# Optimization experiments

Measured on AMD Instinct MI355X. Metric: run time of the kernel, lower is better.

The kernel has to match this reference:

```python
import jax, jax.numpy as jnp
import numpy as np

M, D, I, E, TOPK = 2048, 1024, 2048, 8, 2

def setup_inputs() -> dict:
    key = jax.random.key(0)
    k1, k2, k3, k4 = jax.random.split(key, 4)
    x = jax.random.normal(k1, (M, D), dtype=jnp.float32)
    w13 = jax.random.normal(k2, (E, 2 * I, D), dtype=jnp.float32) * 0.02
    w2 = jax.random.normal(k3, (E, D, I), dtype=jnp.float32) * 0.02
    expert_indices = jax.random.randint(k4, (M, TOPK), 0, E, dtype=jnp.int64)
    return {"x": x, "w13": w13, "w2": w2, "expert_indices": expert_indices}

def reference(x, w13, w2, expert_indices):
    # Faithful to the 'gpt-fast' math: per (token, slot) SiLU-gated expert FFN.
    # Instead of gathering per-token weight copies (huge), compute each expert's
    # FFN densely over all tokens, then gather the selected expert output.
    inter = w2.shape[2]

    def per_expert(w13_e, w2_e):
        h = jnp.einsum('md,nd->mn', x, w13_e)          # [M, 2I]
        x1, x3 = h[:, :inter], h[:, inter:]
        return jnp.einsum('mi,di->md', jax.nn.silu(x1) * x3, w2_e)  # [M, D]

    outs = jax.vmap(per_expert)(w13, w2)               # [E, M, D]
    outs = jnp.transpose(outs, (1, 0, 2))              # [M, E, D]
    # out[t, a] = outs[t, expert_indices[t, a]]
    idx = expert_indices[..., None]                    # [M, TOPK, 1]
    return jnp.take_along_axis(outs, idx, axis=1)      # [M, TOPK, D]
```

## Files before the change

### kernel.cpp

```cpp
#include <hip/hip_runtime.h>
#include <hip/hip_bf16.h>
#include <cstdint>
#include <cstddef>

#define DDIM  1024
#define IDIM  2048
#define NEXP  8
#define NPAIR 4096
#define KSPLIT 2
#define MAXTILE 40

typedef __attribute__((ext_vector_type(8))) short short8;
typedef __attribute__((ext_vector_type(4))) float floatx4;

__device__ inline short8 pack8(float4 a, float4 b) {
    union { short8 s8; __hip_bfloat162 h[4]; } u;
    u.h[0] = __float22bfloat162_rn(float2{a.x, a.y});
    u.h[1] = __float22bfloat162_rn(float2{a.z, a.w});
    u.h[2] = __float22bfloat162_rn(float2{b.x, b.y});
    u.h[3] = __float22bfloat162_rn(float2{b.z, b.w});
    return u.s8;
}

__device__ inline void gload_lds16(const unsigned short* g, unsigned short* l) {
    __builtin_amdgcn_global_load_lds((const __attribute__((address_space(1))) void*)g,
                                     (__attribute__((address_space(3))) void*)l, 16, 0, 0);
}

__global__ void cvt_all(const float4* __restrict__ x, const float4* __restrict__ w13,
                        const float4* __restrict__ w2,
                        uint4* __restrict__ xb, uint4* __restrict__ w13b,
                        uint4* __restrict__ w2b) {
    const int i = blockIdx.x * 256 + threadIdx.x;
    const int NX   = (2048 * 1024) / 8;
    const int NW13 = (8 * 4096 * 1024) / 8;
    const float4* src; uint4* dst; int j;
    if (i < NX)              { src = x;   dst = xb;   j = i; }
    else if (i < NX + NW13)  { src = w13; dst = w13b; j = i - NX; }
    else                     { src = w2;  dst = w2b;  j = i - NX - NW13; }
    float4 a = src[2 * j], b = src[2 * j + 1];
    short8 p = pack8(a, b);
    dst[j] = *(uint4*)&p;
}

__global__ void route_kernel(const int* __restrict__ eidx,
                             int4* __restrict__ tbl,
                             int* __restrict__ slot_q) {
    __shared__ int cnt[NEXP];
    __shared__ int base[NEXP];
    __shared__ int cur[NEXP];
    const int t = threadIdx.x;
    if (t < NEXP) cnt[t] = 0;
    __syncthreads();
    for (int q = t; q < NPAIR; q += 1024) atomicAdd(&cnt[eidx[q]], 1);
    __syncthreads();
    if (t == 0) {
        int s = 0, nt = 0;
        for (int e = 0; e < NEXP; e++) {
            base[e] = s; cur[e] = s;
            for (int mb = 0; mb < cnt[e]; mb += 128)
                tbl[nt++] = int4{e, mb, s, cnt[e]};
            s += cnt[e];
        }
        for (; nt < MAXTILE; nt++) tbl[nt] = int4{0, 0, 0, 0};
    }
    __syncthreads();
    for (int q = t; q < NPAIR; q += 1024) {
        int e = eidx[q];
        int pos = atomicAdd(&cur[e], 1);
        slot_q[pos] = q;
    }
}

__launch_bounds__(256)
__global__ void gemm1_swiglu(const unsigned short* __restrict__ xb,
                             const unsigned short* __restrict__ w13b,
                             const int4* __restrict__ tbl,
                             const int* __restrict__ slot_q,
                             unsigned short* __restrict__ pbuf) {
    const int4 tt = tbl[blockIdx.y];
    const int e = tt.x, mbase = tt.y, off0 = tt.z, ne = tt.w;
    if (mbase >= ne) return;
    const int n0 = blockIdx.x * 64;

    __shared__ __align__(16) unsigned short As[128 * 32];
    __shared__ __align__(16) unsigned short Bs[128 * 32];

    const int t    = threadIdx.x;
    const int lane = t & 63;
    const int wid  = t >> 6;

    const int r0 = t >> 2;
    const int sg = (t & 3) ^ (r0 & 3);
    int slA0 = mbase + r0;      if (slA0 > ne - 1) slA0 = ne - 1;
    int slA1 = mbase + r0 + 64; if (slA1 > ne - 1) slA1 = ne - 1;
    const unsigned short* pA0 = xb + (size_t)(slot_q[off0 + slA0] >> 1) * DDIM + sg * 8;
    const unsigned short* pA1 = xb + (size_t)(slot_q[off0 + slA1] >> 1) * DDIM + sg * 8;
    const unsigned short* wbase = w13b + (size_t)e * (2 * IDIM) * DDIM;
    const unsigned short* pB0 = wbase + (size_t)(n0 + r0) * DDIM + sg * 8;
    const unsigned short* pB1 = wbase + (size_t)(IDIM + n0 + r0) * DDIM + sg * 8;
    unsigned short* lA0 = As + wid * 512;
    unsigned short* lA1 = As + 2048 + wid * 512;
    unsigned short* lB0 = Bs + wid * 512;
    unsigned short* lB1 = Bs + 2048 + wid * 512;

    const int wm = wid >> 1, wn = wid & 1;
    const int quad = lane >> 4, l16 = lane & 15;
    const int swz = (quad ^ (l16 & 3)) * 8;

    floatx4 acc1[4][2], acc3[4][2];
    #pragma unroll
    for (int i = 0; i < 4; i++)
        #pragma unroll
        for (int j = 0; j < 2; j++) {
            acc1[i][j] = floatx4{0.f, 0.f, 0.f, 0.f};
            acc3[i][j] = floatx4{0.f, 0.f, 0.f, 0.f};
        }

    for (int it = 0; it < DDIM / 32; ++it) {
        const int ko = it * 32;
        __syncthreads();
        gload_lds16(pA0 + ko, lA0);
        gload_lds16(pA1 + ko, lA1);
        gload_lds16(pB0 + ko, lB0);
        gload_lds16(pB1 + ko, lB1);
        __syncthreads();

        short8 af[4], b1f[2], b3f[2];
        #pragma unroll
        for (int mi = 0; mi < 4; mi++)
            af[mi] = *(short8*)&As[(wm * 64 + mi * 16 + l16) * 32 + swz];
        #pragma unroll
        for (int ni = 0; ni < 2; ni++) {
            b1f[ni] = *(short8*)&Bs[(wn * 32 + ni * 16 + l16) * 32 + swz];
            b3f[ni] = *(short8*)&Bs[(64 + wn * 32 + ni * 16 + l16) * 32 + swz];
        }
        #pragma unroll
        for (int mi = 0; mi < 4; mi++)
            #pragma unroll
            for (int ni = 0; ni < 2; ni++) {
                acc1[mi][ni] = __builtin_amdgcn_mfma_f32_16x16x32_bf16(af[mi], b1f[ni], acc1[mi][ni], 0, 0, 0);
                acc3[mi][ni] = __builtin_amdgcn_mfma_f32_16x16x32_bf16(af[mi], b3f[ni], acc3[mi][ni], 0, 0, 0);
            }
    }

    #pragma unroll
    for (int mi = 0; mi < 4; mi++) {
        #pragma unroll
        for (int ni = 0; ni < 2; ni++) {
            const int col = n0 + wn * 32 + ni * 16 + l16;
            #pragma unroll
            for (int rr = 0; rr < 4; rr++) {
                const int s2 = mbase + wm * 64 + mi * 16 + quad * 4 + rr;
                if (s2 < ne) {
                    float v1 = acc1[mi][ni][rr];
                    float v3 = acc3[mi][ni][rr];
                    float pv = v1 / (1.f + __expf(-v1)) * v3;
                    __hip_bfloat16 pb = __float2bfloat16(pv);
                    pbuf[(size_t)(off0 + s2) * IDIM + col] = *(unsigned short*)&pb;
                }
            }
        }
    }
}

__launch_bounds__(256)
__global__ void gemm2_scatter(const unsigned short* __restrict__ pbuf,
                              const unsigned short* __restrict__ w2b,
                              const int4* __restrict__ tbl,
                              const int* __restrict__ slot_q,
                              float* __restrict__ out,
                              float* __restrict__ p1) {
    const int4 tt = tbl[blockIdx.y];
    const int e = tt.x, mbase = tt.y, off0 = tt.z, ne = tt.w;
    if (mbase >= ne) return;
    const int n0 = blockIdx.x * 128;
    const int ks = blockIdx.z;
    const int kbase = ks * (IDIM / KSPLIT);

    __shared__ __align__(16) unsigned short As[128 * 32];
    __shared__ __align__(16) unsigned short Bs[128 * 32];

    const int t    = threadIdx.x;
    const int lane = t & 63;
    const int wid  = t >> 6;

    const int r0 = t >> 2;
    const int sg = (t & 3) ^ (r0 & 3);
    int slA0 = mbase + r0;      if (slA0 > ne - 1) slA0 = ne - 1;
    int slA1 = mbase + r0 + 64; if (slA1 > ne - 1) slA1 = ne - 1;
    const unsigned short* pA0 = pbuf + (size_t)(off0 + slA0) * IDIM + kbase + sg * 8;
    const unsigned short* pA1 = pbuf + (size_t)(off0 + slA1) * IDIM + kbase + sg * 8;
    const unsigned short* wbase = w2b + (size_t)e * DDIM * IDIM;
    const unsigned short* pB0 = wbase + (size_t)(n0 + r0) * IDIM + kbase + sg * 8;
    const unsigned short* pB1 = wbase + (size_t)(n0 + 64 + r0) * IDIM + kbase + sg * 8;
    unsigned short* lA0 = As + wid * 512;
    unsigned short* lA1 = As + 2048 + wid * 512;
    unsigned short* lB0 = Bs + wid * 512;
    unsigned short* lB1 = Bs + 2048 + wid * 512;

    const int wm = wid >> 1, wn = wid & 1;
    const int quad = lane >> 4, l16 = lane & 15;
    const int swz = (quad ^ (l16 & 3)) * 8;

    floatx4 acc[4][4];
    #pragma unroll
    for (int i = 0; i < 4; i++)
        #pragma unroll
        for (int j = 0; j < 4; j++) acc[i][j] = floatx4{0.f, 0.f, 0.f, 0.f};

    for (int it = 0; it < (IDIM / KSPLIT) / 32; ++it) {
        const int ko = it * 32;
        __syncthreads();
        gload_lds16(pA0 + ko, lA0);
        gload_lds16(pA1 + ko, lA1);
        gload_lds16(pB0 + ko, lB0);
        gload_lds16(pB1 + ko, lB1);
        __syncthreads();

        short8 af[4], bf[4];
        #pragma unroll
        for (int mi = 0; mi < 4; mi++)
            af[mi] = *(short8*)&As[(wm * 64 + mi * 16 + l16) * 32 + swz];
        #pragma unroll
        for (int ni = 0; ni < 4; ni++)
            bf[ni] = *(short8*)&Bs[(wn * 64 + ni * 16 + l16) * 32 + swz];
        #pragma unroll
        for (int mi = 0; mi < 4; mi++)
            #pragma unroll
            for (int ni = 0; ni < 4; ni++)
                acc[mi][ni] = __builtin_amdgcn_mfma_f32_16x16x32_bf16(af[mi], bf[ni], acc[mi][ni], 0, 0, 0);
    }

    float* dstbase = (ks == 0) ? out : p1;
    #pragma unroll
    for (int mi = 0; mi < 4; mi++) {
        #pragma unroll
        for (int rr = 0; rr < 4; rr++) {
            const int s2 = mbase + wm * 64 + mi * 16 + quad * 4 + rr;
            if (s2 < ne) {
                const int qq = slot_q[off0 + s2];
                float* orow = dstbase + (size_t)qq * DDIM;
                #pragma unroll
                for (int ni = 0; ni < 4; ni++)
                    orow[n0 + wn * 64 + ni * 16 + l16] = acc[mi][ni][rr];
            }
        }
    }
}

__global__ void reduce_add(float4* __restrict__ out, const float4* __restrict__ p1) {
    const int i = blockIdx.x * 256 + threadIdx.x;
    float4 a = out[i], b = p1[i];
    out[i] = float4{a.x + b.x, a.y + b.y, a.z + b.z, a.w + b.w};
}

extern "C" void kernel_launch(void* const* d_in, const int* in_sizes, int n_in,
                              void* d_out, int out_size, void* d_ws, size_t ws_size,
                              hipStream_t stream) {
    const float* x    = (const float*)d_in[0];
    const float* w13  = (const float*)d_in[1];
    const float* w2   = (const float*)d_in[2];
    const int*   eidx = (const int*)d_in[3];
    float* out = (float*)d_out;

    const size_t OFF_XB   = 65536;
    const size_t OFF_W13B = OFF_XB + (size_t)4 * 1024 * 1024;
    const size_t OFF_W2B  = OFF_W13B + (size_t)64 * 1024 * 1024;
    const size_t OFF_PBUF = OFF_W2B + (size_t)32 * 1024 * 1024;

    int4* tbl   = (int4*)((char*)d_ws + 128);
    int* slot_q = (int*)((char*)d_ws + 1024);
    unsigned short* xb   = (unsigned short*)((char*)d_ws + OFF_XB);
    unsigned short* w13b = (unsigned short*)((char*)d_ws + OFF_W13B);
    unsigned short* w2b  = (unsigned short*)((char*)d_ws + OFF_W2B);
    unsigned short* pbuf = (unsigned short*)((char*)d_ws + OFF_PBUF);
    float* p1 = (float*)((char*)d_ws + OFF_W13B);

    hipLaunchKernelGGL(cvt_all, dim3(25600), dim3(256), 0, stream,
                       (const float4*)x, (const float4*)w13, (const float4*)w2,
                       (uint4*)xb, (uint4*)w13b, (uint4*)w2b);
    hipLaunchKernelGGL(route_kernel, dim3(1), dim3(1024), 0, stream, eidx, tbl, slot_q);
    hipLaunchKernelGGL(gemm1_swiglu, dim3(IDIM / 64, MAXTILE), dim3(256), 0, stream,
                       xb, w13b, tbl, slot_q, pbuf);
    hipLaunchKernelGGL(gemm2_scatter, dim3(DDIM / 128, MAXTILE, KSPLIT), dim3(256), 0, stream,
                       pbuf, w2b, tbl, slot_q, out, p1);
    hipLaunchKernelGGL(reduce_add, dim3((NPAIR * DDIM / 4) / 256), dim3(256), 0, stream,
                       (float4*)out, (const float4*)p1);
}
```

Before: 386.2 us.

## Double K-tile depth, raise gemm2 split-K to four, grid-stride nontemporal conversion

Both GEMMs now stage 64-wide K slices per barrier pair instead of 32, with an 8-way XOR swizzle, halving the number of sync/load rounds. The gemm2 split-K goes from 2 to 4 with all partials written to a scratch buffer and summed by a four-way reduce kernel. The fp32-to-bf16 conversion becomes a grid-stride loop with nontemporal loads and two packs per thread, and routing is launched before conversion. The risk is more LDS per block, which lowers occupancy, plus extra partial-sum traffic in the reduce.

```diff
diff --git a/kernel.cpp b/kernel.cpp
--- a/kernel.cpp
+++ b/kernel.cpp
@@ -7,11 +7,12 @@
 #define IDIM  2048
 #define NEXP  8
 #define NPAIR 4096
-#define KSPLIT 2
+#define KSPLIT 4
 #define MAXTILE 40
 
 typedef __attribute__((ext_vector_type(8))) short short8;
 typedef __attribute__((ext_vector_type(4))) float floatx4;
+typedef __attribute__((ext_vector_type(4))) float fvec4;
 
 __device__ inline short8 pack8(float4 a, float4 b) {
     union { short8 s8; __hip_bfloat162 h[4]; } u;
@@ -22,32 +23,49 @@
     return u.s8;
 }
 
+__device__ inline short8 pack8v(fvec4 a, fvec4 b) {
+    union { short8 s8; __hip_bfloat162 h[4]; } u;
+    u.h[0] = __float22bfloat162_rn(float2{a.x, a.y});
+    u.h[1] = __float22bfloat162_rn(float2{a.z, a.w});
+    u.h[2] = __float22bfloat162_rn(float2{b.x, b.y});
+    u.h[3] = __float22bfloat162_rn(float2{b.z, b.w});
+    return u.s8;
+}
+
 __device__ inline void gload_lds16(const unsigned short* g, unsigned short* l) {
     __builtin_amdgcn_global_load_lds((const __attribute__((address_space(1))) void*)g,
                                      (__attribute__((address_space(3))) void*)l, 16, 0, 0);
 }
 
-__global__ void cvt_all(const float4* __restrict__ x, const float4* __restrict__ w13,
-                        const float4* __restrict__ w2,
+__global__ void cvt_all(const fvec4* __restrict__ x, const fvec4* __restrict__ w13,
+                        const fvec4* __restrict__ w2,
                         uint4* __restrict__ xb, uint4* __restrict__ w13b,
                         uint4* __restrict__ w2b) {
-    const int i = blockIdx.x * 256 + threadIdx.x;
     const int NX   = (2048 * 1024) / 8;
     const int NW13 = (8 * 4096 * 1024) / 8;
-    const float4* src; uint4* dst; int j;
-    if (i < NX)              { src = x;   dst = xb;   j = i; }
-    else if (i < NX + NW13)  { src = w13; dst = w13b; j = i - NX; }
-    else                     { src = w2;  dst = w2b;  j = i - NX - NW13; }
-    float4 a = src[2 * j], b = src[2 * j + 1];
-    short8 p = pack8(a, b);
-    dst[j] = *(uint4*)&p;
+    const int NW2  = (8 * 1024 * 2048) / 8;
+    const int total2 = (NX + NW13 + NW2) / 2;
+    for (int i2 = blockIdx.x * 256 + threadIdx.x; i2 < total2; i2 += gridDim.x * 256) {
+        const int i = 2 * i2;
+        const fvec4* src; uint4* dst; int j;
+        if (i < NX)              { src = x;   dst = xb;   j = i; }
+        else if (i < NX + NW13)  { src = w13; dst = w13b; j = i - NX; }
+        else                     { src = w2;  dst = w2b;  j = i - NX - NW13; }
+        fvec4 a0 = __builtin_nontemporal_load(src + 2 * j + 0);
+        fvec4 a1 = __builtin_nontemporal_load(src + 2 * j + 1);
+        fvec4 a2 = __builtin_nontemporal_load(src + 2 * j + 2);
+        fvec4 a3 = __builtin_nontemporal_load(src + 2 * j + 3);
+        short8 p0 = pack8v(a0, a1);
+        short8 p1 = pack8v(a2, a3);
+        dst[j]     = *(uint4*)&p0;
+        dst[j + 1] = *(uint4*)&p1;
+    }
 }
 
 __global__ void route_kernel(const int* __restrict__ eidx,
                              int4* __restrict__ tbl,
                              int* __restrict__ slot_q) {
     __shared__ int cnt[NEXP];
-    __shared__ int base[NEXP];
     __shared__ int cur[NEXP];
     const int t = threadIdx.x;
     if (t < NEXP) cnt[t] = 0;
@@ -57,7 +75,7 @@
     if (t == 0) {
         int s = 0, nt = 0;
         for (int e = 0; e < NEXP; e++) {
-            base[e] = s; cur[e] = s;
+            cur[e] = s;
             for (int mb = 0; mb < cnt[e]; mb += 128)
                 tbl[nt++] = int4{e, mb, s, cnt[e]};
             s += cnt[e];
@@ -83,30 +101,34 @@
     if (mbase >= ne) return;
     const int n0 = blockIdx.x * 64;
 
-    __shared__ __align__(16) unsigned short As[128 * 32];
-    __shared__ __align__(16) unsigned short Bs[128 * 32];
+    __shared__ __align__(16) unsigned short As[128 * 64];
+    __shared__ __align__(16) unsigned short Bs[128 * 64];
 
     const int t    = threadIdx.x;
     const int lane = t & 63;
     const int wid  = t >> 6;
 
-    const int r0 = t >> 2;
-    const int sg = (t & 3) ^ (r0 & 3);
-    int slA0 = mbase + r0;      if (slA0 > ne - 1) slA0 = ne - 1;
-    int slA1 = mbase + r0 + 64; if (slA1 > ne - 1) slA1 = ne - 1;
-    const unsigned short* pA0 = xb + (size_t)(slot_q[off0 + slA0] >> 1) * DDIM + sg * 8;
-    const unsigned short* pA1 = xb + (size_t)(slot_q[off0 + slA1] >> 1) * DDIM + sg * 8;
-    const unsigned short* wbase = w13b + (size_t)e * (2 * IDIM) * DDIM;
-    const unsigned short* pB0 = wbase + (size_t)(n0 + r0) * DDIM + sg * 8;
-    const unsigned short* pB1 = wbase + (size_t)(IDIM + n0 + r0) * DDIM + sg * 8;
-    unsigned short* lA0 = As + wid * 512;
-    unsigned short* lA1 = As + 2048 + wid * 512;
-    unsigned short* lB0 = Bs + wid * 512;
-    unsigned short* lB1 = Bs + 2048 + wid * 512;
+    const int rr = t >> 3;
+    const int g  = (t & 7) ^ (rr & 7);
+    const unsigned short* pA[4];
+    const unsigned short* pB[4];
+    const unsigned short* wb1 = w13b + (size_t)e * (2 * IDIM) * DDIM;
+    #pragma unroll
+    for (int c = 0; c < 4; c++) {
+        int row = c * 32 + rr;
+        int sl = mbase + row; if (sl > ne - 1) sl = ne - 1;
+        pA[c] = xb + (size_t)(slot_q[off0 + sl] >> 1) * DDIM + g * 8;
+        int wrow = (row < 64) ? (n0 + row) : (IDIM + n0 + (row - 64));
+        pB[c] = wb1 + (size_t)wrow * DDIM + g * 8;
+    }
+    unsigned short* lA = As + wid * 512;
+    unsigned short* lB = Bs + wid * 512;
 
     const int wm = wid >> 1, wn = wid & 1;
     const int quad = lane >> 4, l16 = lane & 15;
-    const int swz = (quad ^ (l16 & 3)) * 8;
+    const int rsw = l16 & 7;
+    const int co0 = (quad ^ rsw) * 8;
+    const int co1 = ((quad + 4) ^ rsw) * 8;
 
     floatx4 acc1[4][2], acc3[4][2];
     #pragma unroll
@@ -117,31 +139,36 @@
             acc3[i][j] = floatx4{0.f, 0.f, 0.f, 0.f};
         }
 
-    for (int it = 0; it < DDIM / 32; ++it) {
-        const int ko = it * 32;
+    for (int it = 0; it < DDIM / 64; ++it) {
+        const int ko = it * 64;
         __syncthreads();
-        gload_lds16(pA0 + ko, lA0);
-        gload_lds16(pA1 + ko, lA1);
-        gload_lds16(pB0 + ko, lB0);
-        gload_lds16(pB1 + ko, lB1);
+        #pragma unroll
+        for (int c = 0; c < 4; c++) {
+            gload_lds16(pA[c] + ko, lA + c * 2048);
+            gload_lds16(pB[c] + ko, lB + c * 2048);
+        }
         __syncthreads();
 
-        short8 af[4], b1f[2], b3f[2];
-        #pragma unroll
-        for (int mi = 0; mi < 4; mi++)
-            af[mi] = *(short8*)&As[(wm * 64 + mi * 16 + l16) * 32 + swz];
-        #pragma unroll
-        for (int ni = 0; ni < 2; ni++) {
-            b1f[ni] = *(short8*)&Bs[(wn * 32 + ni * 16 + l16) * 32 + swz];
-            b3f[ni] = *(short8*)&Bs[(64 + wn * 32 + ni * 16 + l16) * 32 + swz];
-        }
-        #pragma unroll
-        for (int mi = 0; mi < 4; mi++)
+        #pragma unroll
+        for (int h = 0; h < 2; ++h) {
+            const int co = h ? co1 : co0;
+            short8 af[4], b1f[2], b3f[2];
+            #pragma unroll
+            for (int mi = 0; mi < 4; mi++)
+                af[mi] = *(short8*)&As[(wm * 64 + mi * 16 + l16) * 64 + co];
             #pragma unroll
             for (int ni = 0; ni < 2; ni++) {
-                acc1[mi][ni] = __builtin_amdgcn_mfma_f32_16x16x32_bf16(af[mi], b1f[ni], acc1[mi][ni], 0, 0, 0);
-                acc3[mi][ni] = __builtin_amdgcn_mfma_f32_16x16x32_bf16(af[mi], b3f[ni], acc3[mi][ni], 0, 0, 0);
+                b1f[ni] = *(short8*)&Bs[(wn * 32 + ni * 16 + l16) * 64 + co];
+                b3f[ni] = *(short8*)&Bs[(64 + wn * 32 + ni * 16 + l16) * 64 + co];
             }
+            #pragma unroll
+            for (int mi = 0; mi < 4; mi++)
+                #pragma unroll
+                for (int ni = 0; ni < 2; ni++) {
+                    acc1[mi][ni] = __builtin_amdgcn_mfma_f32_16x16x32_bf16(af[mi], b1f[ni], acc1[mi][ni], 0, 0, 0);
+                    acc3[mi][ni] = __builtin_amdgcn_mfma_f32_16x16x32_bf16(af[mi], b3f[ni], acc3[mi][ni], 0, 0, 0);
+                }
+        }
     }
 
     #pragma unroll
@@ -150,11 +177,11 @@
         for (int ni = 0; ni < 2; ni++) {
             const int col = n0 + wn * 32 + ni * 16 + l16;
             #pragma unroll
-            for (int rr = 0; rr < 4; rr++) {
-                const int s2 = mbase + wm * 64 + mi * 16 + quad * 4 + rr;
+            for (int rw = 0; rw < 4; rw++) {
+                const int s2 = mbase + wm * 64 + mi * 16 + quad * 4 + rw;
                 if (s2 < ne) {
-                    float v1 = acc1[mi][ni][rr];
-                    float v3 = acc3[mi][ni][rr];
+                    float v1 = acc1[mi][ni][rw];
+                    float v3 = acc3[mi][ni][rw];
                     float pv = v1 / (1.f + __expf(-v1)) * v3;
                     __hip_bfloat16 pb = __float2bfloat16(pv);
                     pbuf[(size_t)(off0 + s2) * IDIM + col] = *(unsigned short*)&pb;
@@ -169,39 +196,41 @@
                               const unsigned short* __restrict__ w2b,
                               const int4* __restrict__ tbl,
                               const int* __restrict__ slot_q,
-                              float* __restrict__ out,
-                              float* __restrict__ p1) {
+                              float* __restrict__ parts) {
     const int4 tt = tbl[blockIdx.y];
     const int e = tt.x, mbase = tt.y, off0 = tt.z, ne = tt.w;
     if (mbase >= ne) return;
     const int n0 = blockIdx.x * 128;
-    const int ks = blockIdx.z;
-    const int kbase = ks * (IDIM / KSPLIT);
-
-    __shared__ __align__(16) unsigned short As[128 * 32];
-    __shared__ __align__(16) unsigned short Bs[128 * 32];
+    const int kbase = blockIdx.z * (IDIM / KSPLIT);
+    float* dstbase = parts + (size_t)blockIdx.z * NPAIR * DDIM;
+
+    __shared__ __align__(16) unsigned short As[128 * 64];
+    __shared__ __align__(16) unsigned short Bs[128 * 64];
 
     const int t    = threadIdx.x;
     const int lane = t & 63;
     const int wid  = t >> 6;
 
-    const int r0 = t >> 2;
-    const int sg = (t & 3) ^ (r0 & 3);
-    int slA0 = mbase + r0;      if (slA0 > ne - 1) slA0 = ne - 1;
-    int slA1 = mbase + r0 + 64; if (slA1 > ne - 1) slA1 = ne - 1;
-    const unsigned short* pA0 = pbuf + (size_t)(off0 + slA0) * IDIM + kbase + sg * 8;
-    const unsigned short* pA1 = pbuf + (size_t)(off0 + slA1) * IDIM + kbase + sg * 8;
-    const unsigned short* wbase = w2b + (size_t)e * DDIM * IDIM;
-    const unsigned short* pB0 = wbase + (size_t)(n0 + r0) * IDIM + kbase + sg * 8;
-    const unsigned short* pB1 = wbase + (size_t)(n0 + 64 + r0) * IDIM + kbase + sg * 8;
-    unsigned short* lA0 = As + wid * 512;
-    unsigned short* lA1 = As + 2048 + wid * 512;
-    unsigned short* lB0 = Bs + wid * 512;
-    unsigned short* lB1 = Bs + 2048 + wid * 512;
+    const int rr = t >> 3;
+    const int g  = (t & 7) ^ (rr & 7);
+    const unsigned short* pA[4];
+    const unsigned short* pB[4];
+    const unsigned short* wb = w2b + (size_t)e * DDIM * IDIM;
+    #pragma unroll
+    for (int c = 0; c < 4; c++) {
+        int row = c * 32 + rr;
+        int sl = mbase + row; if (sl > ne - 1) sl = ne - 1;
+        pA[c] = pbuf + (size_t)(off0 + sl) * IDIM + kbase + g * 8;
+        pB[c] = wb + (size_t)(n0 + row) * IDIM + kbase + g * 8;
+    }
+    unsigned short* lA = As + wid * 512;
+    unsigned short* lB = Bs + wid * 512;
 
     const int wm = wid >> 1, wn = wid & 1;
     const int quad = lane >> 4, l16 = lane & 15;
-    const int swz = (quad ^ (l16 & 3)) * 8;
+    const int rsw = l16 & 7;
+    const int co0 = (quad ^ rsw) * 8;
+    const int co1 = ((quad + 4) ^ rsw) * 8;
 
     floatx4 acc[4][4];
     #pragma unroll
@@ -209,50 +238,57 @@
         #pragma unroll
         for (int j = 0; j < 4; j++) acc[i][j] = floatx4{0.f, 0.f, 0.f, 0.f};
 
-    for (int it = 0; it < (IDIM / KSPLIT) / 32; ++it) {
-        const int ko = it * 32;
+    for (int it = 0; it < (IDIM / KSPLIT) / 64; ++it) {
+        const int ko = it * 64;
         __syncthreads();
-        gload_lds16(pA0 + ko, lA0);
-        gload_lds16(pA1 + ko, lA1);
-        gload_lds16(pB0 + ko, lB0);
-        gload_lds16(pB1 + ko, lB1);
+        #pragma unroll
+        for (int c = 0; c < 4; c++) {
+            gload_lds16(pA[c] + ko, lA + c * 2048);
+            gload_lds16(pB[c] + ko, lB + c * 2048);
+        }
         __syncthreads();
 
-        short8 af[4], bf[4];
-        #pragma unroll
-        for (int mi = 0; mi < 4; mi++)
-            af[mi] = *(short8*)&As[(wm * 64 + mi * 16 + l16) * 32 + swz];
-        #pragma unroll
-        for (int ni = 0; ni < 4; ni++)
-            bf[ni] = *(short8*)&Bs[(wn * 64 + ni * 16 + l16) * 32 + swz];
-        #pragma unroll
-        for (int mi = 0; mi < 4; mi++)
+        #pragma unroll
+        for (int h = 0; h < 2; ++h) {
+            const int co = h ? co1 : co0;
+            short8 af[4], bf[4];
+            #pragma unroll
+            for (int mi = 0; mi < 4; mi++)
+                af[mi] = *(short8*)&As[(wm * 64 + mi * 16 + l16) * 64 + co];
             #pragma unroll
             for (int ni = 0; ni < 4; ni++)
-                acc[mi][ni] = __builtin_amdgcn_mfma_f32_16x16x32_bf16(af[mi], bf[ni], acc[mi][ni], 0, 0, 0);
-    }
-
-    float* dstbase = (ks == 0) ? out : p1;
+                bf[ni] = *(short8*)&Bs[(wn * 64 + ni * 16 + l16) * 64 + co];
+            #pragma unroll
+            for (int mi = 0; mi < 4; mi++)
+                #pragma unroll
+                for (int ni = 0; ni < 4; ni++)
+                    acc[mi][ni] = __builtin_amdgcn_mfma_f32_16x16x32_bf16(af[mi], bf[ni], acc[mi][ni], 0, 0, 0);
+        }
+    }
+
     #pragma unroll
     for (int mi = 0; mi < 4; mi++) {
         #pragma unroll
-        for (int rr = 0; rr < 4; rr++) {
-            const int s2 = mbase + wm * 64 + mi * 16 + quad * 4 + rr;
+        for (int rw = 0; rw < 4; rw++) {
+            const int s2 = mbase + wm * 64 + mi * 16 + quad * 4 + rw;
             if (s2 < ne) {
                 const int qq = slot_q[off0 + s2];
                 float* orow = dstbase + (size_t)qq * DDIM;
                 #pragma unroll
                 for (int ni = 0; ni < 4; ni++)
-                    orow[n0 + wn * 64 + ni * 16 + l16] = acc[mi][ni][rr];
+                    orow[n0 + wn * 64 + ni * 16 + l16] = acc[mi][ni][rw];
             }
         }
     }
 }
 
-__global__ void reduce_add(float4* __restrict__ out, const float4* __restrict__ p1) {
+__global__ void reduce_add4(float4* __restrict__ out, const float4* __restrict__ parts) {
     const int i = blockIdx.x * 256 + threadIdx.x;
-    float4 a = out[i], b = p1[i];
-    out[i] = float4{a.x + b.x, a.y + b.y, a.z + b.z, a.w + b.w};
+    const int stride = NPAIR * DDIM / 4;
+    float4 a = parts[i], b = parts[i + stride];
+    float4 c = parts[i + 2 * stride], d = parts[i + 3 * stride];
+    out[i] = float4{a.x + b.x + c.x + d.x, a.y + b.y + c.y + d.y,
+                    a.z + b.z + c.z + d.z, a.w + b.w + c.w + d.w};
 }
 
 extern "C" void kernel_launch(void* const* d_in, const int* in_sizes, int n_in,
@@ -275,16 +311,16 @@
     unsigned short* w13b = (unsigned short*)((char*)d_ws + OFF_W13B);
     unsigned short* w2b  = (unsigned short*)((char*)d_ws + OFF_W2B);
     unsigned short* pbuf = (unsigned short*)((char*)d_ws + OFF_PBUF);
-    float* p1 = (float*)((char*)d_ws + OFF_W13B);
-
-    hipLaunchKernelGGL(cvt_all, dim3(25600), dim3(256), 0, stream,
-                       (const float4*)x, (const float4*)w13, (const float4*)w2,
+    float* parts = (float*)((char*)d_ws + OFF_W13B);
+
+    hipLaunchKernelGGL(route_kernel, dim3(1), dim3(1024), 0, stream, eidx, tbl, slot_q);
+    hipLaunchKernelGGL(cvt_all, dim3(2048), dim3(256), 0, stream,
+                       (const fvec4*)x, (const fvec4*)w13, (const fvec4*)w2,
                        (uint4*)xb, (uint4*)w13b, (uint4*)w2b);
-    hipLaunchKernelGGL(route_kernel, dim3(1), dim3(1024), 0, stream, eidx, tbl, slot_q);
     hipLaunchKernelGGL(gemm1_swiglu, dim3(IDIM / 64, MAXTILE), dim3(256), 0, stream,
                        xb, w13b, tbl, slot_q, pbuf);
     hipLaunchKernelGGL(gemm2_scatter, dim3(DDIM / 128, MAXTILE, KSPLIT), dim3(256), 0, stream,
-                       pbuf, w2b, tbl, slot_q, out, p1);
-    hipLaunchKernelGGL(reduce_add, dim3((NPAIR * DDIM / 4) / 256), dim3(256), 0, stream,
-                       (float4*)out, (const float4*)p1);
-}
+                       pbuf, w2b, tbl, slot_q, parts);
+    hipLaunchKernelGGL(reduce_add4, dim3((NPAIR * DDIM / 4) / 256), dim3(256), 0, stream,
+                       (float4*)out, (const float4*)parts);
+}
```

Result: no change. 383.7 us (-0.6%).
